# Optimization experiments

Measured on AMD Instinct MI355X. Metric: run time of the kernel, lower is better.

## Reference

```python
import jax, jax.numpy as jnp
import numpy as np

NUM_CLASSES = 21
SMOOTH = 1e-06


def setup_inputs() -> dict:
    key = jax.random.key(0)
    k1, k2 = jax.random.split(key)
    pred = jax.random.normal(k1, (8, NUM_CLASSES, 512, 512), dtype=jnp.float32)
    target = jax.random.randint(k2, (8, 512, 512), 0, NUM_CLASSES, dtype=jnp.int32)
    return {"pred": pred, "target": target}


def reference(pred, target):
    # softmax over class dim then argmax -> hard label map [B, H, W]
    probs = jax.nn.softmax(pred, axis=1)
    pred_lbl = jnp.argmax(probs, axis=1)

    pf = pred_lbl.reshape(-1).astype(jnp.int32)
    tf = target.reshape(-1).astype(jnp.int32)

    # Fused confusion-histogram pass: per-class counts in one traversal each.
    cnt_pred = jnp.bincount(pf, length=NUM_CLASSES)
    cnt_tgt = jnp.bincount(tf, length=NUM_CLASSES)
    # intersection_c = #{pred==c & target==c}; route mismatches to overflow bin C
    inter = jnp.bincount(jnp.where(pf == tf, pf, NUM_CLASSES), length=NUM_CLASSES + 1)[:NUM_CLASSES]

    inter = inter.astype(jnp.float32)
    union = (cnt_pred + cnt_tgt).astype(jnp.float32) - inter  # |A|+|B|-|A&B|

    iou = (inter + SMOOTH) / (union + SMOOTH)
    return jnp.mean(iou)
```

## Files before the change

### kernel.cpp

```cpp
#include <hip/hip_runtime.h>

#define NUM_CLASSES 21
#define HW (512 * 512)
#define NBATCH 8
#define TOTAL_PIX (NBATCH * HW)
#define SMOOTH 1e-6f


__global__ void iou_hist_kernel(const float* __restrict__ pred,
                                const int* __restrict__ target,
                                unsigned int* __restrict__ counts) {
    __shared__ unsigned int s_pi[NUM_CLASSES];
    __shared__ unsigned int s_tgt[NUM_CLASSES];

    const int tid = threadIdx.x;
    if (tid < NUM_CLASSES) {
        s_pi[tid] = 0u;
        s_tgt[tid] = 0u;
    }
    __syncthreads();

    const int q = blockIdx.x * blockDim.x + tid;
    const int p = q * 4;
    const int b = p / HW;
    const int i = p - b * HW;
    const float* base = pred + (size_t)b * NUM_CLASSES * HW + i;

    float4 w[NUM_CLASSES];
#pragma unroll
    for (int c = 0; c < NUM_CLASSES; ++c) {
        w[c] = *reinterpret_cast<const float4*>(base + (size_t)c * HW);
    }

    float bv0 = w[0].x, bv1 = w[0].y, bv2 = w[0].z, bv3 = w[0].w;
    int bi0 = 0, bi1 = 0, bi2 = 0, bi3 = 0;
#pragma unroll
    for (int c = 1; c < NUM_CLASSES; ++c) {
        if (w[c].x > bv0) { bv0 = w[c].x; bi0 = c; }
        if (w[c].y > bv1) { bv1 = w[c].y; bi1 = c; }
        if (w[c].z > bv2) { bv2 = w[c].z; bi2 = c; }
        if (w[c].w > bv3) { bv3 = w[c].w; bi3 = c; }
    }

    int4 t = *reinterpret_cast<const int4*>(target + p);

    atomicAdd(&s_pi[bi0], 1u + (bi0 == t.x ? 0x10000u : 0u));
    atomicAdd(&s_pi[bi1], 1u + (bi1 == t.y ? 0x10000u : 0u));
    atomicAdd(&s_pi[bi2], 1u + (bi2 == t.z ? 0x10000u : 0u));
    atomicAdd(&s_pi[bi3], 1u + (bi3 == t.w ? 0x10000u : 0u));

    atomicAdd(&s_tgt[t.x], 1u);
    atomicAdd(&s_tgt[t.y], 1u);
    atomicAdd(&s_tgt[t.z], 1u);
    atomicAdd(&s_tgt[t.w], 1u);

    __syncthreads();
    if (tid < NUM_CLASSES) {
        unsigned int pi = s_pi[tid];
        unsigned int ct = s_tgt[tid];
        if (pi & 0xFFFFu) atomicAdd(&counts[tid], pi & 0xFFFFu);
        if (ct) atomicAdd(&counts[NUM_CLASSES + tid], ct);
        if (pi >> 16) atomicAdd(&counts[2 * NUM_CLASSES + tid], pi >> 16);
    }
}

__global__ void iou_finalize_kernel(const unsigned int* __restrict__ counts,
                                    float* __restrict__ out) {
    const int c = threadIdx.x;
    float iou = 0.0f;
    if (c < NUM_CLASSES) {
        float inter = (float)counts[2 * NUM_CLASSES + c];
        float uni = (float)counts[c] + (float)counts[NUM_CLASSES + c] - inter;
        iou = (inter + SMOOTH) / (uni + SMOOTH);
    }
#pragma unroll
    for (int off = 32; off > 0; off >>= 1) iou += __shfl_down(iou, off);
    if (c == 0) out[0] = iou * (1.0f / NUM_CLASSES);
}

extern "C" void kernel_launch(void* const* d_in, const int* in_sizes, int n_in,
                              void* d_out, int out_size, void* d_ws, size_t ws_size,
                              hipStream_t stream) {
    const float* pred = (const float*)d_in[0];
    const int* target = (const int*)d_in[1];
    float* out = (float*)d_out;
    unsigned int* counts = (unsigned int*)d_ws;

    hipMemsetAsync(counts, 0, 3 * NUM_CLASSES * sizeof(unsigned int), stream);

    const int nquads = TOTAL_PIX / 4;
    const int block = 256;
    const int grid = nquads / block;
    iou_hist_kernel<<<grid, block, 0, stream>>>(pred, target, counts);
    iou_finalize_kernel<<<1, 64, 0, stream>>>(counts, out);
}
```

Before: 261.1 us.

## Replace global atomics with per-block partial histograms and two-stage reduction

The histogram kernel now handles 2 pixels per thread with float2 loads, so it runs 4096 blocks instead of 2048. Each block writes its 63 counters to a class-major partial buffer instead of doing global atomics. This removes the memset and the global atomic contention. A per-class reduction kernel sums the partials and computes IoU, and a final kernel averages the classes. The trade-offs are narrower loads, an extra kernel launch and an extra partial-buffer round trip.

```diff
diff --git a/kernel.cpp b/kernel.cpp
--- a/kernel.cpp
+++ b/kernel.cpp
@@ -5,77 +5,94 @@
 #define NBATCH 8
 #define TOTAL_PIX (NBATCH * HW)
 #define SMOOTH 1e-6f
+#define NBLK 4096
 
 
-__global__ void iou_hist_kernel(const float* __restrict__ pred,
-                                const int* __restrict__ target,
-                                unsigned int* __restrict__ counts) {
+__global__ __launch_bounds__(256) void iou_hist(const float* __restrict__ pred,
+                                                const int* __restrict__ target,
+                                                unsigned int* __restrict__ part) {
     __shared__ unsigned int s_pi[NUM_CLASSES];
     __shared__ unsigned int s_tgt[NUM_CLASSES];
 
     const int tid = threadIdx.x;
-    if (tid < NUM_CLASSES) {
-        s_pi[tid] = 0u;
-        s_tgt[tid] = 0u;
-    }
+    if (tid < NUM_CLASSES) { s_pi[tid] = 0u; s_tgt[tid] = 0u; }
     __syncthreads();
 
-    const int q = blockIdx.x * blockDim.x + tid;
-    const int p = q * 4;
-    const int b = p / HW;
-    const int i = p - b * HW;
-    const float* base = pred + (size_t)b * NUM_CLASSES * HW + i;
+    const int q = blockIdx.x * 256 + tid;
+    const int p = q * 2;
+    const int b = p >> 18;
+    const int i = p & (HW - 1);
+    const float* base = pred + (((size_t)b * NUM_CLASSES) << 18) + i;
 
-    float4 w[NUM_CLASSES];
+    float2 w[NUM_CLASSES];
 #pragma unroll
-    for (int c = 0; c < NUM_CLASSES; ++c) {
-        w[c] = *reinterpret_cast<const float4*>(base + (size_t)c * HW);
-    }
+    for (int c = 0; c < NUM_CLASSES; ++c)
+        w[c] = *reinterpret_cast<const float2*>(base + ((size_t)c << 18));
 
-    float bv0 = w[0].x, bv1 = w[0].y, bv2 = w[0].z, bv3 = w[0].w;
-    int bi0 = 0, bi1 = 0, bi2 = 0, bi3 = 0;
+    float bv0 = w[0].x, bv1 = w[0].y;
+    int bi0 = 0, bi1 = 0;
 #pragma unroll
     for (int c = 1; c < NUM_CLASSES; ++c) {
         if (w[c].x > bv0) { bv0 = w[c].x; bi0 = c; }
         if (w[c].y > bv1) { bv1 = w[c].y; bi1 = c; }
-        if (w[c].z > bv2) { bv2 = w[c].z; bi2 = c; }
-        if (w[c].w > bv3) { bv3 = w[c].w; bi3 = c; }
     }
 
-    int4 t = *reinterpret_cast<const int4*>(target + p);
+    int2 t = *reinterpret_cast<const int2*>(target + p);
 
     atomicAdd(&s_pi[bi0], 1u + (bi0 == t.x ? 0x10000u : 0u));
     atomicAdd(&s_pi[bi1], 1u + (bi1 == t.y ? 0x10000u : 0u));
-    atomicAdd(&s_pi[bi2], 1u + (bi2 == t.z ? 0x10000u : 0u));
-    atomicAdd(&s_pi[bi3], 1u + (bi3 == t.w ? 0x10000u : 0u));
-
     atomicAdd(&s_tgt[t.x], 1u);
     atomicAdd(&s_tgt[t.y], 1u);
-    atomicAdd(&s_tgt[t.z], 1u);
-    atomicAdd(&s_tgt[t.w], 1u);
 
     __syncthreads();
     if (tid < NUM_CLASSES) {
         unsigned int pi = s_pi[tid];
-        unsigned int ct = s_tgt[tid];
-        if (pi & 0xFFFFu) atomicAdd(&counts[tid], pi & 0xFFFFu);
-        if (ct) atomicAdd(&counts[NUM_CLASSES + tid], ct);
-        if (pi >> 16) atomicAdd(&counts[2 * NUM_CLASSES + tid], pi >> 16);
+        part[(0 * NUM_CLASSES + tid) * NBLK + blockIdx.x] = pi & 0xFFFFu;
+        part[(1 * NUM_CLASSES + tid) * NBLK + blockIdx.x] = s_tgt[tid];
+        part[(2 * NUM_CLASSES + tid) * NBLK + blockIdx.x] = pi >> 16;
     }
 }
 
-__global__ void iou_finalize_kernel(const unsigned int* __restrict__ counts,
-                                    float* __restrict__ out) {
-    const int c = threadIdx.x;
-    float iou = 0.0f;
-    if (c < NUM_CLASSES) {
-        float inter = (float)counts[2 * NUM_CLASSES + c];
-        float uni = (float)counts[c] + (float)counts[NUM_CLASSES + c] - inter;
-        iou = (inter + SMOOTH) / (uni + SMOOTH);
+__global__ __launch_bounds__(256) void iou_reduce1(const unsigned int* __restrict__ part,
+                                                   float* __restrict__ iou_parts) {
+    const int c = blockIdx.x;
+    const int tid = threadIdx.x;
+    const uint4* p0 = reinterpret_cast<const uint4*>(part + (0 * NUM_CLASSES + c) * NBLK);
+    const uint4* p1 = reinterpret_cast<const uint4*>(part + (1 * NUM_CLASSES + c) * NBLK);
+    const uint4* p2 = reinterpret_cast<const uint4*>(part + (2 * NUM_CLASSES + c) * NBLK);
+
+    unsigned int s0 = 0, s1 = 0, s2 = 0;
+#pragma unroll
+    for (int k = tid; k < NBLK / 4; k += 256) {
+        uint4 a = p0[k]; s0 += a.x + a.y + a.z + a.w;
+        uint4 bb = p1[k]; s1 += bb.x + bb.y + bb.z + bb.w;
+        uint4 d = p2[k]; s2 += d.x + d.y + d.z + d.w;
     }
 #pragma unroll
-    for (int off = 32; off > 0; off >>= 1) iou += __shfl_down(iou, off);
-    if (c == 0) out[0] = iou * (1.0f / NUM_CLASSES);
+    for (int off = 32; off > 0; off >>= 1) {
+        s0 += __shfl_down(s0, off);
+        s1 += __shfl_down(s1, off);
+        s2 += __shfl_down(s2, off);
+    }
+    __shared__ unsigned int ls[3][4];
+    const int w = tid >> 6, lane = tid & 63;
+    if (lane == 0) { ls[0][w] = s0; ls[1][w] = s1; ls[2][w] = s2; }
+    __syncthreads();
+    if (tid == 0) {
+        unsigned int t0 = ls[0][0] + ls[0][1] + ls[0][2] + ls[0][3];
+        unsigned int t1 = ls[1][0] + ls[1][1] + ls[1][2] + ls[1][3];
+        unsigned int t2 = ls[2][0] + ls[2][1] + ls[2][2] + ls[2][3];
+        float inter = (float)t2;
+        float uni = (float)t0 + (float)t1 - inter;
+        iou_parts[c] = (inter + SMOOTH) / (uni + SMOOTH);
+    }
+}
+
+__global__ void iou_reduce2(const float* __restrict__ iou_parts, float* __restrict__ out) {
+    float v = threadIdx.x < NUM_CLASSES ? iou_parts[threadIdx.x] : 0.0f;
+#pragma unroll
+    for (int off = 32; off > 0; off >>= 1) v += __shfl_down(v, off);
+    if (threadIdx.x == 0) out[0] = v * (1.0f / NUM_CLASSES);
 }
 
 extern "C" void kernel_launch(void* const* d_in, const int* in_sizes, int n_in,
@@ -84,13 +101,11 @@
     const float* pred = (const float*)d_in[0];
     const int* target = (const int*)d_in[1];
     float* out = (float*)d_out;
-    unsigned int* counts = (unsigned int*)d_ws;
 
-    hipMemsetAsync(counts, 0, 3 * NUM_CLASSES * sizeof(unsigned int), stream);
+    unsigned int* part = (unsigned int*)d_ws;
+    float* iou_parts = (float*)(part + 3 * NUM_CLASSES * NBLK);
 
-    const int nquads = TOTAL_PIX / 4;
-    const int block = 256;
-    const int grid = nquads / block;
-    iou_hist_kernel<<<grid, block, 0, stream>>>(pred, target, counts);
-    iou_finalize_kernel<<<1, 64, 0, stream>>>(counts, out);
+    iou_hist<<<NBLK, 256, 0, stream>>>(pred, target, part);
+    iou_reduce1<<<NUM_CLASSES, 256, 0, stream>>>(part, iou_parts);
+    iou_reduce2<<<1, 64, 0, stream>>>(iou_parts, out);
 }
```

New measurement: 245.5 us. 1.06x faster.
